# Kernel optimization log

Hardware: AMD Instinct MI355X
Metric: run time of the kernel (lower is better)

## Reference

```python
import jax, jax.numpy as jnp
import numpy as np

N, F, D, H = 8192, 128, 128, 2
LEAKY_ALPHA = 0.3  # keras.layers.LeakyReLU default


def setup_inputs() -> dict:
    key = jax.random.key(0)
    ks = jax.random.split(key, 8)
    x = jax.random.normal(ks[0], (N, F), dtype=jnp.float32)
    # sparse-ish binary adjacency with self loops, stored dense (as the module does)
    adj = (jax.random.uniform(ks[1], (N, N)) < 0.01).astype(jnp.float32)
    adj = jnp.clip(adj + jnp.eye(N, dtype=jnp.float32), 0.0, 1.0)
    s = 1.0 / np.sqrt(F)
    Wmap = jax.random.normal(ks[2], (H, F, D), dtype=jnp.float32) * s
    a1_w = jax.random.normal(ks[3], (H, D), dtype=jnp.float32) * (1.0 / np.sqrt(D))
    a2_w = jax.random.normal(ks[4], (H, D), dtype=jnp.float32) * (1.0 / np.sqrt(D))
    a1_b = jnp.zeros((H,), dtype=jnp.float32)
    a2_b = jnp.zeros((H,), dtype=jnp.float32)
    kernel = jax.random.normal(ks[5], (H, F, D), dtype=jnp.float32) * s
    bias = jnp.zeros((H, N, D), dtype=jnp.float32)
    return {"x": x, "adj": adj, "Wmap": Wmap, "a1_w": a1_w, "a1_b": a1_b,
            "a2_w": a2_w, "a2_b": a2_b, "kernel": kernel, "bias": bias}


def reference(x, adj, Wmap, a1_w, a1_b, a2_w, a2_b, kernel, bias):
    # per-head Conv1D(k=1, no bias): node-wise linear map  [H, N, D]
    mapped = jnp.einsum('nf,hfd->hnd', x, Wmap)
    # per-head Conv1D(k=1) scalar scores  [H, N]
    sa1 = jnp.einsum('hnd,hd->hn', mapped, a1_w) + a1_b[:, None]
    sa2 = jnp.einsum('hnd,hd->hn', mapped, a2_w) + a2_b[:, None]
    # additive score masked multiplicatively by adjacency:  [H, N, N]
    w = adj[None, :, :] * sa1[:, :, None] + adj[None, :, :] * sa2[:, None, :]
    w = jnp.where(w >= 0, w, LEAKY_ALPHA * w)
    att = jax.nn.softmax(w, axis=-1)  # softmax over neighbors (incl. zeroed entries, as in source)
    value = jnp.einsum('nf,hfd->hnd', x, kernel)
    out = jnp.einsum('hnm,hmd->hnd', att, value) + bias  # [H, N, D]
    return out.mean(axis=0)  # attn_heads_reduction='average', linear activation
```

## Files before the change

### kernel.cpp

```cpp
#include <hip/hip_runtime.h>
#include <hip/hip_bf16.h>

#define NN 8192
#define FF 128
#define DD 128
#define HH 2
#define ALPHA 0.3f
#define MAXNNZ 1024

__global__ __launch_bounds__(256) void c_kernel(
    const float* __restrict__ Wmap, const float* __restrict__ a1w,
    const float* __restrict__ a2w, float* __restrict__ c1, float* __restrict__ c2) {
  int t = threadIdx.x;
  int h = t >> 7, f = t & 127;
  const float* wrow = Wmap + ((size_t)h * FF + f) * DD;
  const float* a1 = a1w + h * DD;
  const float* a2 = a2w + h * DD;
  float s1 = 0.f, s2 = 0.f;
  #pragma unroll 8
  for (int d = 0; d < DD; d++) {
    float w = wrow[d];
    s1 += w * a1[d];
    s2 += w * a2[d];
  }
  c1[t] = s1;
  c2[t] = s2;
}

__global__ __launch_bounds__(128) void sa_kernel(
    const float* __restrict__ x, const float* __restrict__ c1,
    const float* __restrict__ c2, const float* __restrict__ a1b,
    const float* __restrict__ a2b, float* __restrict__ sa1, float* __restrict__ sa2) {
  int n = blockIdx.x;
  int f = threadIdx.x;
  float xv = x[(size_t)n * FF + f];
  float p00 = xv * c1[f];
  float p01 = xv * c1[FF + f];
  float p10 = xv * c2[f];
  float p11 = xv * c2[FF + f];
  #pragma unroll
  for (int o = 32; o > 0; o >>= 1) {
    p00 += __shfl_down(p00, o);
    p01 += __shfl_down(p01, o);
    p10 += __shfl_down(p10, o);
    p11 += __shfl_down(p11, o);
  }
  __shared__ float part[2][4];
  int w = f >> 6;
  if ((f & 63) == 0) {
    part[w][0] = p00; part[w][1] = p01; part[w][2] = p10; part[w][3] = p11;
  }
  __syncthreads();
  if (f == 0) {
    sa1[n]      = part[0][0] + part[1][0] + a1b[0];
    sa1[NN + n] = part[0][1] + part[1][1] + a1b[1];
    sa2[n]      = part[0][2] + part[1][2] + a2b[0];
    sa2[NN + n] = part[0][3] + part[1][3] + a2b[1];
  }
}

__global__ __launch_bounds__(256) void value_gemm(
    const float* __restrict__ x, const float* __restrict__ kern,
    unsigned short* __restrict__ value_bf, float* __restrict__ colsum) {
  int h = blockIdx.y;
  int row0 = blockIdx.x * 32;
  __shared__ float Bl[64 * 128];
  __shared__ float Al[32 * 129];
  const float4* Bg4 = (const float4*)(kern + (size_t)h * FF * DD);
  const float4* Ag4 = (const float4*)(x + (size_t)row0 * FF);
  float4* Bl4 = (float4*)Bl;
  int tid = threadIdx.x;

  #pragma unroll
  for (int q = 0; q < 4; q++) {
    int idx = q * 256 + tid;
    int r = idx >> 5, c4 = idx & 31;
    float4 g = Ag4[idx];
    Al[r * 129 + c4 * 4 + 0] = g.x;
    Al[r * 129 + c4 * 4 + 1] = g.y;
    Al[r * 129 + c4 * 4 + 2] = g.z;
    Al[r * 129 + c4 * 4 + 3] = g.w;
  }

  int cg = tid & 31;
  int rg = tid >> 5;
  float4 acc[4];
  #pragma unroll
  for (int m = 0; m < 4; m++) acc[m] = make_float4(0.f, 0.f, 0.f, 0.f);

  for (int kp = 0; kp < 2; kp++) {
    __syncthreads();
    #pragma unroll
    for (int q = 0; q < 8; q++)
      Bl4[q * 256 + tid] = Bg4[kp * 2048 + q * 256 + tid];
    __syncthreads();
    for (int k2 = 0; k2 < 64; k2++) {
      int k = kp * 64 + k2;
      float4 bv = *(const float4*)&Bl[k2 * 128 + cg * 4];
      #pragma unroll
      for (int m = 0; m < 4; m++) {
        float av = Al[(rg + m * 8) * 129 + k];
        acc[m].x += av * bv.x;
        acc[m].y += av * bv.y;
        acc[m].z += av * bv.z;
        acc[m].w += av * bv.w;
      }
    }
  }

  #pragma unroll
  for (int m = 0; m < 4; m++) {
    int r = row0 + rg + m * 8;
    ushort4 pk;
    __hip_bfloat16 b0 = __float2bfloat16(acc[m].x);
    __hip_bfloat16 b1 = __float2bfloat16(acc[m].y);
    __hip_bfloat16 b2 = __float2bfloat16(acc[m].z);
    __hip_bfloat16 b3 = __float2bfloat16(acc[m].w);
    pk.x = *(unsigned short*)&b0;
    pk.y = *(unsigned short*)&b1;
    pk.z = *(unsigned short*)&b2;
    pk.w = *(unsigned short*)&b3;
    *(ushort4*)&value_bf[((size_t)h * NN + r) * DD + cg * 4] = pk;
  }

  float4 cp;
  cp.x = acc[0].x + acc[1].x + acc[2].x + acc[3].x;
  cp.y = acc[0].y + acc[1].y + acc[2].y + acc[3].y;
  cp.z = acc[0].z + acc[1].z + acc[2].z + acc[3].z;
  cp.w = acc[0].w + acc[1].w + acc[2].w + acc[3].w;
  __syncthreads();
  float* colred = Al;
  *(float4*)&colred[rg * 128 + cg * 4] = cp;
  __syncthreads();
  if (rg == 0) {
    #pragma unroll
    for (int c = 0; c < 4; c++) {
      int col = cg * 4 + c;
      float s = 0.f;
      #pragma unroll
      for (int rr = 0; rr < 8; rr++) s += colred[rr * 128 + col];
      atomicAdd(&colsum[h * DD + col], s);
    }
  }
}

__global__ __launch_bounds__(256) void gat_main(
    const float* __restrict__ adj, const float* __restrict__ sa1,
    const float* __restrict__ sa2, const unsigned short* __restrict__ value_bf,
    const float* __restrict__ colsum, const float* __restrict__ bias,
    float* __restrict__ out) {
  int i = blockIdx.x;
  __shared__ int idxbuf[MAXNNZ];
  __shared__ float em1buf[HH][MAXNNZ];
  __shared__ int cnt;
  __shared__ float sume_sh[HH];
  __shared__ float wred[4][HH];
  __shared__ float contrib[256];
  int t = threadIdx.x;
  int lane = t & 63;
  if (t == 0) cnt = 0;
  __syncthreads();

  const float4* arow = (const float4*)(adj + (size_t)i * NN);
  #pragma unroll
  for (int q = 0; q < 8; q++) {
    int f4 = q * 256 + t;
    float4 a = arow[f4];
    int j0 = f4 * 4;
    float av[4] = {a.x, a.y, a.z, a.w};
    #pragma unroll
    for (int c = 0; c < 4; c++) {
      bool nz = (av[c] != 0.f);
      unsigned long long m = __ballot(nz);
      int tot = __popcll(m);
      int base = 0;
      if (lane == 0 && tot) base = atomicAdd(&cnt, tot);
      base = __shfl(base, 0);
      if (nz) {
        int p = base + __popcll(m & ((1ull << lane) - 1ull));
        if (p < MAXNNZ) idxbuf[p] = j0 + c;
      }
    }
  }
  __syncthreads();
  int count = min(cnt, MAXNNZ);

  float s10 = sa1[i];
  float s11 = sa1[NN + i];
  float l0 = 0.f, l1 = 0.f;
  for (int k = t; k < count; k += 256) {
    int j = idxbuf[k];
    float w0 = s10 + sa2[j];
    float w1 = s11 + sa2[NN + j];
    w0 = (w0 >= 0.f) ? w0 : ALPHA * w0;
    w1 = (w1 >= 0.f) ? w1 : ALPHA * w1;
    float e0 = __expf(w0) - 1.f;
    float e1 = __expf(w1) - 1.f;
    em1buf[0][k] = e0;
    em1buf[1][k] = e1;
    l0 += e0;
    l1 += e1;
  }
  #pragma unroll
  for (int o = 32; o > 0; o >>= 1) {
    l0 += __shfl_down(l0, o);
    l1 += __shfl_down(l1, o);
  }
  int wid = t >> 6;
  if (lane == 0) { wred[wid][0] = l0; wred[wid][1] = l1; }
  __syncthreads();
  if (t == 0) {
    sume_sh[0] = wred[0][0] + wred[1][0] + wred[2][0] + wred[3][0];
    sume_sh[1] = wred[0][1] + wred[1][1] + wred[2][1] + wred[3][1];
  }
  __syncthreads();

  int h = t >> 7, d = t & 127;
  const unsigned short* val = value_bf + (size_t)h * NN * DD + d;
  const float* eb = em1buf[h];
  float acc = 0.f;
  #pragma unroll 4
  for (int k = 0; k < count; k++) {
    int j = idxbuf[k];
    unsigned short u = val[(size_t)j * DD];
    __hip_bfloat16 bv = *(__hip_bfloat16*)&u;
    acc += eb[k] * __bfloat162float(bv);
  }
  float denom = (float)NN + sume_sh[h];
  float r = (colsum[h * DD + d] + acc) / denom +
            bias[((size_t)h * NN + i) * DD + d];
  contrib[t] = r;
  __syncthreads();
  if (t < 64) {
    float2 o2;
    o2.x = 0.5f * (contrib[2 * t]     + contrib[2 * t + 128]);
    o2.y = 0.5f * (contrib[2 * t + 1] + contrib[2 * t + 129]);
    *(float2*)&out[(size_t)i * DD + 2 * t] = o2;
  }
}

extern "C" void kernel_launch(void* const* d_in, const int* in_sizes, int n_in,
                              void* d_out, int out_size, void* d_ws, size_t ws_size,
                              hipStream_t stream) {
  const float* x    = (const float*)d_in[0];
  const float* adj  = (const float*)d_in[1];
  const float* Wmap = (const float*)d_in[2];
  const float* a1w  = (const float*)d_in[3];
  const float* a1b  = (const float*)d_in[4];
  const float* a2w  = (const float*)d_in[5];
  const float* a2b  = (const float*)d_in[6];
  const float* kern = (const float*)d_in[7];
  const float* bias = (const float*)d_in[8];
  float* out = (float*)d_out;
  float* ws  = (float*)d_ws;

  float* c1     = ws;
  float* c2     = ws + 256;
  float* sa1    = ws + 512;
  float* sa2    = ws + 16896;
  float* colsum = ws + 33280;
  unsigned short* value_bf = (unsigned short*)(ws + 33536);

  hipMemsetAsync(colsum, 0, HH * DD * sizeof(float), stream);
  c_kernel<<<1, 256, 0, stream>>>(Wmap, a1w, a2w, c1, c2);
  sa_kernel<<<NN, 128, 0, stream>>>(x, c1, c2, a1b, a2b, sa1, sa2);
  value_gemm<<<dim3(NN / 32, HH), 256, 0, stream>>>(x, kern, value_bf, colsum);
  gat_main<<<NN, 256, 0, stream>>>(adj, sa1, sa2, value_bf, colsum, bias, out);
}
```

Measured before the change: 468.1 us.

## Fuse score prep into value GEMM and stream adjacency with nontemporal loads

Folds the c-vector computation and the per-node attention score kernel into the value GEMM kernel, so each block recomputes its head's c vector and scores its 32 rows from the x tile already in shared memory. This cuts the launch sequence from four kernels to two. The adjacency and bias reads in the main kernel now use nontemporal loads to avoid polluting cache with single-use data. In exchange, every block redundantly recomputes the Wmap·a dot products and gets a little longer before its GEMM starts.

```diff
diff --git a/kernel.cpp b/kernel.cpp
--- a/kernel.cpp
+++ b/kernel.cpp
@@ -8,64 +8,19 @@
 #define ALPHA 0.3f
 #define MAXNNZ 1024
 
-__global__ __launch_bounds__(256) void c_kernel(
+typedef float vfloat4 __attribute__((ext_vector_type(4)));
+
+__global__ __launch_bounds__(256) void prep_kernel(
+    const float* __restrict__ x, const float* __restrict__ kern,
     const float* __restrict__ Wmap, const float* __restrict__ a1w,
-    const float* __restrict__ a2w, float* __restrict__ c1, float* __restrict__ c2) {
-  int t = threadIdx.x;
-  int h = t >> 7, f = t & 127;
-  const float* wrow = Wmap + ((size_t)h * FF + f) * DD;
-  const float* a1 = a1w + h * DD;
-  const float* a2 = a2w + h * DD;
-  float s1 = 0.f, s2 = 0.f;
-  #pragma unroll 8
-  for (int d = 0; d < DD; d++) {
-    float w = wrow[d];
-    s1 += w * a1[d];
-    s2 += w * a2[d];
-  }
-  c1[t] = s1;
-  c2[t] = s2;
-}
-
-__global__ __launch_bounds__(128) void sa_kernel(
-    const float* __restrict__ x, const float* __restrict__ c1,
-    const float* __restrict__ c2, const float* __restrict__ a1b,
-    const float* __restrict__ a2b, float* __restrict__ sa1, float* __restrict__ sa2) {
-  int n = blockIdx.x;
-  int f = threadIdx.x;
-  float xv = x[(size_t)n * FF + f];
-  float p00 = xv * c1[f];
-  float p01 = xv * c1[FF + f];
-  float p10 = xv * c2[f];
-  float p11 = xv * c2[FF + f];
-  #pragma unroll
-  for (int o = 32; o > 0; o >>= 1) {
-    p00 += __shfl_down(p00, o);
-    p01 += __shfl_down(p01, o);
-    p10 += __shfl_down(p10, o);
-    p11 += __shfl_down(p11, o);
-  }
-  __shared__ float part[2][4];
-  int w = f >> 6;
-  if ((f & 63) == 0) {
-    part[w][0] = p00; part[w][1] = p01; part[w][2] = p10; part[w][3] = p11;
-  }
-  __syncthreads();
-  if (f == 0) {
-    sa1[n]      = part[0][0] + part[1][0] + a1b[0];
-    sa1[NN + n] = part[0][1] + part[1][1] + a1b[1];
-    sa2[n]      = part[0][2] + part[1][2] + a2b[0];
-    sa2[NN + n] = part[0][3] + part[1][3] + a2b[1];
-  }
-}
-
-__global__ __launch_bounds__(256) void value_gemm(
-    const float* __restrict__ x, const float* __restrict__ kern,
-    unsigned short* __restrict__ value_bf, float* __restrict__ colsum) {
+    const float* __restrict__ a2w, const float* __restrict__ a1b,
+    const float* __restrict__ a2b, unsigned short* __restrict__ value_bf,
+    float* __restrict__ colsum, float* __restrict__ sa1, float* __restrict__ sa2) {
   int h = blockIdx.y;
   int row0 = blockIdx.x * 32;
   __shared__ float Bl[64 * 128];
   __shared__ float Al[32 * 129];
+  __shared__ float cvec[2][128];
   const float4* Bg4 = (const float4*)(kern + (size_t)h * FF * DD);
   const float4* Ag4 = (const float4*)(x + (size_t)row0 * FF);
   float4* Bl4 = (float4*)Bl;
@@ -80,6 +35,32 @@
     Al[r * 129 + c4 * 4 + 1] = g.y;
     Al[r * 129 + c4 * 4 + 2] = g.z;
     Al[r * 129 + c4 * 4 + 3] = g.w;
+  }
+
+  {
+    int which = tid >> 7, f = tid & 127;
+    const float4* w4 = (const float4*)(Wmap + ((size_t)h * FF + f) * DD);
+    const float4* av4 = (const float4*)((which ? a2w : a1w) + (size_t)h * DD);
+    float s = 0.f;
+    #pragma unroll 8
+    for (int dq = 0; dq < 32; dq++) {
+      float4 w = w4[dq];
+      float4 a = av4[dq];
+      s += w.x * a.x + w.y * a.y + w.z * a.z + w.w * a.w;
+    }
+    cvec[which][f] = s;
+  }
+  __syncthreads();
+
+  if (tid < 64) {
+    int r = tid & 31, type = tid >> 5;
+    const float* cv = cvec[type];
+    float s = 0.f;
+    #pragma unroll 8
+    for (int f = 0; f < 128; f++) s += Al[r * 129 + f] * cv[f];
+    float b = type ? a2b[h] : a1b[h];
+    float* dst = type ? sa2 : sa1;
+    dst[(size_t)h * NN + row0 + r] = s + b;
   }
 
   int cg = tid & 31;
@@ -161,16 +142,15 @@
   if (t == 0) cnt = 0;
   __syncthreads();
 
-  const float4* arow = (const float4*)(adj + (size_t)i * NN);
+  const vfloat4* arow = (const vfloat4*)(adj + (size_t)i * NN);
   #pragma unroll
   for (int q = 0; q < 8; q++) {
     int f4 = q * 256 + t;
-    float4 a = arow[f4];
+    vfloat4 a = __builtin_nontemporal_load(&arow[f4]);
     int j0 = f4 * 4;
-    float av[4] = {a.x, a.y, a.z, a.w};
     #pragma unroll
     for (int c = 0; c < 4; c++) {
-      bool nz = (av[c] != 0.f);
+      bool nz = (a[c] != 0.f);
       unsigned long long m = __ballot(nz);
       int tot = __popcll(m);
       int base = 0;
@@ -227,8 +207,8 @@
     acc += eb[k] * __bfloat162float(bv);
   }
   float denom = (float)NN + sume_sh[h];
-  float r = (colsum[h * DD + d] + acc) / denom +
-            bias[((size_t)h * NN + i) * DD + d];
+  float bb = __builtin_nontemporal_load(&bias[((size_t)h * NN + i) * DD + d]);
+  float r = (colsum[h * DD + d] + acc) / denom + bb;
   contrib[t] = r;
   __syncthreads();
   if (t < 64) {
@@ -254,16 +234,13 @@
   float* out = (float*)d_out;
   float* ws  = (float*)d_ws;
 
-  float* c1     = ws;
-  float* c2     = ws + 256;
-  float* sa1    = ws + 512;
-  float* sa2    = ws + 16896;
-  float* colsum = ws + 33280;
-  unsigned short* value_bf = (unsigned short*)(ws + 33536);
-
-  hipMemsetAsync(colsum, 0, HH * DD * sizeof(float), stream);
-  c_kernel<<<1, 256, 0, stream>>>(Wmap, a1w, a2w, c1, c2);
-  sa_kernel<<<NN, 128, 0, stream>>>(x, c1, c2, a1b, a2b, sa1, sa2);
-  value_gemm<<<dim3(NN / 32, HH), 256, 0, stream>>>(x, kern, value_bf, colsum);
+  float* sa1    = ws;
+  float* sa2    = ws + 16384;
+  float* colsum = ws + 32768;
+  unsigned short* value_bf = (unsigned short*)(ws + 33024);
+
+  (void)hipMemsetAsync(colsum, 0, HH * DD * sizeof(float), stream);
+  prep_kernel<<<dim3(NN / 32, HH), 256, 0, stream>>>(
+      x, kern, Wmap, a1w, a2w, a1b, a2b, value_bf, colsum, sa1, sa2);
   gat_main<<<NN, 256, 0, stream>>>(adj, sa1, sa2, value_bf, colsum, bias, out);
 }
```

Result: no change. 460.6 us (-1.6%).
